# Performance work log

Measured on AMD Instinct MI355X. Metric: run time of the kernel, lower is better.

## Reference

```python
import jax, jax.numpy as jnp
import numpy as np

# ---- model hyperparameters (match init_kwargs) ----
D_MODEL = 1024
D_STATE = 128
EXPAND = 2
HEADDIM = 64
NGROUPS = 1
D_INNER = EXPAND * D_MODEL            # 2048
NHEADS = D_INNER // HEADDIM           # 32
ROPE_FRAC = 0.5
SPLIT = int(D_STATE * ROPE_FRAC)      # 64 rotary dims
NANG = SPLIT // 2                     # 32 rope angles
A_FLOOR = 1e-4
EPS = 1e-5
BATCH, SEQLEN = 1, 1024
SIZES = [D_INNER, D_INNER, D_STATE * NGROUPS, D_STATE * NGROUPS, NHEADS, NHEADS, NHEADS, NANG]
D_IN_PROJ = int(np.sum(SIZES))        # 4480


def setup_inputs() -> dict:
    key = jax.random.key(0)
    ks = jax.random.split(key, 6)
    u = jax.random.normal(ks[0], (BATCH, SEQLEN, D_MODEL), dtype=jnp.float32)
    W_in = jax.random.normal(ks[1], (D_MODEL, D_IN_PROJ), dtype=jnp.float32) * 0.02
    # dt_bias ~ log(dt) for dt in [1e-3, 0.1] -> around -4
    dt_bias = jax.random.normal(ks[2], (NHEADS,), dtype=jnp.float32) * 0.5 - 4.0
    B_bias = jnp.ones((NHEADS, D_STATE), jnp.float32) + 0.01 * jax.random.normal(ks[3], (NHEADS, D_STATE), dtype=jnp.float32)
    C_bias = jnp.ones((NHEADS, D_STATE), jnp.float32) + 0.01 * jax.random.normal(ks[4], (NHEADS, D_STATE), dtype=jnp.float32)
    Bn_w = jnp.ones((D_STATE,), jnp.float32)
    Cn_w = jnp.ones((D_STATE,), jnp.float32)
    D_param = jnp.ones((NHEADS,), jnp.float32)
    W_out = jax.random.normal(ks[5], (D_INNER, D_MODEL), dtype=jnp.float32) * 0.02
    return {"u": u, "W_in": W_in, "dt_bias": dt_bias, "B_bias": B_bias, "C_bias": C_bias,
            "Bn_w": Bn_w, "Cn_w": Cn_w, "D_param": D_param, "W_out": W_out}


def _rmsnorm(v, w):
    return v * jax.lax.rsqrt(jnp.mean(v * v, axis=-1, keepdims=True) + EPS) * w


def _forward(u, W_in, dt_bias, B_bias, C_bias, Bn_w, Cn_w, D_param, W_out):
    b, l, _ = u.shape
    proj = u @ W_in                                   # (b, l, d_in_proj)
    idx = np.cumsum(SIZES)[:-1]
    z, x, Bp, Cp, dd_dt, dd_A, trap_raw, ang = jnp.split(proj, idx, axis=-1)
    z = z.reshape(b, l, NHEADS, HEADDIM)
    x = x.reshape(b, l, NHEADS, HEADDIM)
    # A = clamp(-softplus(.), max=-A_floor);  dt = softplus(. + dt_bias)
    A = jnp.minimum(-jax.nn.softplus(dd_A), -A_FLOOR)          # (b,l,H)
    dt = jax.nn.softplus(dd_dt + dt_bias)                      # (b,l,H)
    a = jnp.exp(A * dt)                                        # decay per step
    lam = jax.nn.sigmoid(trap_raw)                             # trapezoid gate
    # RMSNorm on B/C (ngroups=1), then per-head additive bias
    Bn = _rmsnorm(Bp, Bn_w)                                    # (b,l,N)
    Cn = _rmsnorm(Cp, Cn_w)
    Bh = Bn[:, :, None, :] + B_bias                            # (b,l,H,N)
    Ch = Cn[:, :, None, :] + C_bias
    # data-dependent rotary: cumulative angle = cumsum(angles * dt)
    theta = jnp.cumsum(ang[:, :, None, :] * dt[..., None], axis=1)  # (b,l,H,NANG)
    cos, sin = jnp.cos(theta), jnp.sin(theta)

    def rope(v):
        d1, d2, rest = v[..., :NANG], v[..., NANG:SPLIT], v[..., SPLIT:]
        return jnp.concatenate([d1 * cos - d2 * sin, d1 * sin + d2 * cos, rest], axis=-1)

    Bh, Ch = rope(Bh), rope(Ch)

    tfirst = lambda v: jnp.moveaxis(v, 1, 0)
    inputs = (tfirst(Bh), tfirst(Ch), tfirst(x), tfirst(a), tfirst(dt), tfirst(lam))
    h0 = jnp.zeros((b, NHEADS, HEADDIM, D_STATE), jnp.float32)
    k0 = jnp.zeros((b, NHEADS, D_STATE), jnp.float32)
    v0 = jnp.zeros((b, NHEADS, HEADDIM), jnp.float32)

    def step(carry, inp):
        h, kp, vp = carry
        Bt, Ct, xt, at, dtt, lamt = inp
        # trapezoidal selective-scan update:
        # h_t = a_t h_{t-1} + dt_t (lam_t B_t x_t + (1-lam_t) a_t B_{t-1} x_{t-1})
        cur = jnp.einsum('bhp,bhn->bhpn', xt, Bt) * (dtt * lamt)[..., None, None]
        prv = jnp.einsum('bhp,bhn->bhpn', vp, kp) * (dtt * (1.0 - lamt) * at)[..., None, None]
        h = at[..., None, None] * h + cur + prv
        yt = jnp.einsum('bhn,bhpn->bhp', Ct, h)
        return (h, Bt, xt), yt

    _, y = jax.lax.scan(step, (h0, k0, v0), inputs)          # (l,b,H,P)
    y = jnp.moveaxis(y, 0, 1) + D_param[None, None, :, None] * x
    y = y * jax.nn.silu(z)                                    # gated output (no out-proj norm)
    return y.reshape(b, l, D_INNER) @ W_out


def reference(u, W_in, dt_bias, B_bias, C_bias, Bn_w, Cn_w, D_param, W_out):
    return _forward(u, W_in, dt_bias, B_bias, C_bias, Bn_w, Cn_w, D_param, W_out)
```

## Files before the change

kernel.cpp:

```cpp
#include <hip/hip_runtime.h>
#include <stdint.h>

#define SEQ     1024
#define DPROJ   4480

typedef __attribute__((ext_vector_type(8))) short short8;
typedef __attribute__((ext_vector_type(4))) float f4;

__device__ __forceinline__ short f2b(float f){
  union { float f; uint32_t u; } v; v.f = f;
  uint32_t r = (v.u + 0x7fffu + ((v.u >> 16) & 1u)) >> 16;
  return (short)(uint16_t)r;
}
__device__ __forceinline__ float b2f(uint16_t u){
  union { uint32_t u; float f; } v; v.u = ((uint32_t)u) << 16; return v.f;
}
__device__ __forceinline__ uint32_t pack2(float lo, float hi){
  return (uint32_t)(uint16_t)f2b(lo) | ((uint32_t)(uint16_t)f2b(hi) << 16);
}
__device__ __forceinline__ float softplus_f(float x){
  return x > 20.f ? x : log1pf(__expf(x));
}
__device__ __forceinline__ void gload_lds16(const short* g, short* l){
  __builtin_amdgcn_global_load_lds((const __attribute__((address_space(1))) void*)g,
                                   (__attribute__((address_space(3))) void*)l, 16, 0, 0);
}

__global__ __launch_bounds__(256) void cast_kernel(const float* __restrict__ in, short* __restrict__ out){
  int i = (blockIdx.x * 256 + threadIdx.x) * 4;
  f4 v = *(const f4*)(in + i);
  uint2 pk; pk.x = pack2(v.x, v.y); pk.y = pack2(v.z, v.w);
  *(uint2*)(out + i) = pk;
}

__global__ __launch_bounds__(256) void transpose_cast(const float* __restrict__ in, short* __restrict__ out,
                                                      int R, int C, int lda, int c0){
  __shared__ float tile[32][33];
  int bc = blockIdx.x * 32;
  int br = blockIdx.y * 32;
  int tx = threadIdx.x, ty = threadIdx.y;
  #pragma unroll
  for (int i = 0; i < 32; i += 8)
    tile[ty + i][tx] = in[(size_t)(br + ty + i) * lda + c0 + bc + tx];
  __syncthreads();
  #pragma unroll
  for (int i = 0; i < 32; i += 8)
    out[(size_t)(bc + ty + i) * R + br + tx] = f2b(tile[tx][ty + i]);
}

__global__ __launch_bounds__(256) void gemm_bt(const short* __restrict__ A, const short* __restrict__ Bt,
                                               float* __restrict__ C, int M, int N, int K, int klen){
  __shared__ __align__(16) short As[128 * 32];
  __shared__ __align__(16) short Bs[128 * 32];
  const int tid  = threadIdx.x;
  const int wave = tid >> 6;
  const int lane = tid & 63;
  const int m0 = blockIdx.y * 128;
  const int n0 = blockIdx.x * 128;
  const int k0 = blockIdx.z * klen;
  C += (size_t)blockIdx.z * M * N;
  const int wm = (wave >> 1) * 64;
  const int wn = (wave & 1) * 64;
  const int quad = lane >> 4;
  const int r16  = lane & 15;

  f4 acc[4][4];
  #pragma unroll
  for (int i = 0; i < 4; i++)
    #pragma unroll
    for (int j = 0; j < 4; j++) acc[i][j] = (f4){0.f, 0.f, 0.f, 0.f};

  const int row0 = tid >> 2;
  const int kq   = tid & 3;
  const short* gA0 = A  + (size_t)(m0 + row0) * K + k0 + kq * 8;
  const short* gA1 = A  + (size_t)(m0 + row0 + 64) * K + k0 + kq * 8;
  const short* gB0 = Bt + (size_t)(n0 + row0) * K + k0 + kq * 8;
  const short* gB1 = Bt + (size_t)(n0 + row0 + 64) * K + k0 + kq * 8;
  short* lA0 = &As[(size_t)tid * 8];
  short* lA1 = &As[(size_t)(tid + 256) * 8];
  short* lB0 = &Bs[(size_t)tid * 8];
  short* lB1 = &Bs[(size_t)(tid + 256) * 8];

  const int nk = klen >> 5;
  for (int kt = 0; kt < nk; ++kt){
    const int ko = kt * 32;
    __syncthreads();
    gload_lds16(gA0 + ko, lA0);
    gload_lds16(gA1 + ko, lA1);
    gload_lds16(gB0 + ko, lB0);
    gload_lds16(gB1 + ko, lB1);
    __syncthreads();
    short8 af[4], bf[4];
    #pragma unroll
    for (int i = 0; i < 4; i++){
      af[i] = *(const short8*)&As[(wm + i * 16 + r16) * 32 + quad * 8];
      bf[i] = *(const short8*)&Bs[(wn + i * 16 + r16) * 32 + quad * 8];
    }
    #pragma unroll
    for (int i = 0; i < 4; i++)
      #pragma unroll
      for (int j = 0; j < 4; j++)
        acc[i][j] = __builtin_amdgcn_mfma_f32_16x16x32_bf16(af[i], bf[j], acc[i][j], 0, 0, 0);
  }

  #pragma unroll
  for (int i = 0; i < 4; i++)
    #pragma unroll
    for (int j = 0; j < 4; j++)
      #pragma unroll
      for (int rr = 0; rr < 4; ++rr){
        int row = m0 + wm + i * 16 + quad * 4 + rr;
        int col = n0 + wn + j * 16 + r16;
        C[(size_t)row * N + col] = acc[i][j][rr];
      }
}

__global__ __launch_bounds__(256) void reduce4_kernel(const float* __restrict__ p, float* __restrict__ out){
  int i = (blockIdx.x * 256 + threadIdx.x) * 4;
  f4 a = *(const f4*)(p + i);
  f4 b = *(const f4*)(p + 1048576 + i);
  f4 c = *(const f4*)(p + 2097152 + i);
  f4 d = *(const f4*)(p + 3145728 + i);
  f4 s; s.x = (a.x + b.x) + (c.x + d.x); s.y = (a.y + b.y) + (c.y + d.y);
  s.z = (a.z + b.z) + (c.z + d.z); s.w = (a.w + b.w) + (c.w + d.w);
  *(f4*)(out + i) = s;
}

__global__ __launch_bounds__(256) void prep_kernel(const float* __restrict__ proj,
                                                   const float* __restrict__ dt_bias,
                                                   f4* __restrict__ coefA){
  int idx = blockIdx.x * 256 + threadIdx.x;
  int t = idx >> 5, h = idx & 31;
  const float* row = proj + (size_t)t * DPROJ;
  float dt  = softplus_f(row[4352 + h] + dt_bias[h]);
  float Ah  = -fmaxf(softplus_f(row[4384 + h]), 1e-4f);
  float lam = 1.f / (1.f + __expf(-row[4416 + h]));
  f4 c; c.x = Ah * dt; c.y = dt * lam; c.z = dt * (1.f - lam); c.w = dt;
  coefA[idx] = c;
}

__global__ __launch_bounds__(256) void scanL_kernel(const f4* __restrict__ coefA,
                                                    float* __restrict__ Lcum,
                                                    float* __restrict__ u2b,
                                                    float* __restrict__ c1b){
  int h = blockIdx.x;
  int tid = threadIdx.x;
  int t0 = tid * 4;
  float v[4], c1[4], c2n[4];
  #pragma unroll
  for (int i = 0; i < 4; i++){
    f4 cc = coefA[(t0 + i) * 32 + h];
    v[i] = cc.x; c1[i] = cc.y;
  }
  #pragma unroll
  for (int i = 0; i < 4; i++){
    int t = t0 + i;
    c2n[i] = (t < 1023) ? coefA[(t + 1) * 32 + h].z : 0.f;
  }
  v[1] += v[0]; v[2] += v[1]; v[3] += v[2];
  float tot = v[3], sc = tot;
  int lane = tid & 63, wave = tid >> 6;
  #pragma unroll
  for (int off = 1; off < 64; off <<= 1){
    float n = __shfl_up(sc, off, 64);
    if (lane >= off) sc += n;
  }
  __shared__ float wsum[4];
  if (lane == 63) wsum[wave] = sc;
  __syncthreads();
  float base = sc - tot;
  for (int w = 0; w < wave; ++w) base += wsum[w];
  #pragma unroll
  for (int i = 0; i < 4; i++){
    int t = t0 + i;
    Lcum[h * 1024 + t] = base + v[i];
    u2b[h * 1024 + t]  = c1[i] + c2n[i];
    c1b[h * 1024 + t]  = c1[i];
  }
}

__global__ __launch_bounds__(256) void theta2_kernel(const float* __restrict__ proj,
                                                     const f4* __restrict__ coefA,
                                                     float* __restrict__ cosb, float* __restrict__ sinb){
  int h = blockIdx.x >> 5, k = blockIdx.x & 31;
  int tid = threadIdx.x;
  int t0 = tid * 4;
  float v[4];
  #pragma unroll
  for (int i = 0; i < 4; i++){
    int t = t0 + i;
    v[i] = proj[(size_t)t * DPROJ + 4448 + k] * coefA[t * 32 + h].w;
  }
  v[1] += v[0]; v[2] += v[1]; v[3] += v[2];
  float tot = v[3], sc = tot;
  int lane = tid & 63, wave = tid >> 6;
  #pragma unroll
  for (int off = 1; off < 64; off <<= 1){
    float n = __shfl_up(sc, off, 64);
    if (lane >= off) sc += n;
  }
  __shared__ float wsum[4];
  if (lane == 63) wsum[wave] = sc;
  __syncthreads();
  float base = sc - tot;
  for (int w = 0; w < wave; ++w) base += wsum[w];
  #pragma unroll
  for (int i = 0; i < 4; i++){
    float th = base + v[i];
    float s, c;
    __sincosf(th, &s, &c);
    int t = t0 + i;
    cosb[(size_t)t * 1024 + h * 32 + k] = c;
    sinb[(size_t)t * 1024 + h * 32 + k] = s;
  }
}

__global__ __launch_bounds__(256) void bc_kernel(const float* __restrict__ proj,
                                                 const float* __restrict__ B_bias, const float* __restrict__ C_bias,
                                                 const float* __restrict__ Bn_w, const float* __restrict__ Cn_w,
                                                 const float* __restrict__ cosb, const float* __restrict__ sinb,
                                                 short* __restrict__ Bb, short* __restrict__ Cb){
  int t = blockIdx.x;
  int tid = threadIdx.x;
  __shared__ float vB[128], vC[128];
  __shared__ float red[4];
  int n = tid & 127;
  bool isC = tid >= 128;
  float val = proj[(size_t)t * DPROJ + 4096 + (isC ? 128 : 0) + n];
  float ss = val * val;
  #pragma unroll
  for (int off = 32; off >= 1; off >>= 1) ss += __shfl_down(ss, off);
  int wave = tid >> 6, lane = tid & 63;
  if (lane == 0) red[wave] = ss;
  __syncthreads();
  float rsv = isC ? rsqrtf((red[2] + red[3]) * (1.f / 128.f) + 1e-5f)
                  : rsqrtf((red[0] + red[1]) * (1.f / 128.f) + 1e-5f);
  float nv = val * rsv * (isC ? Cn_w[n] : Bn_w[n]);
  (isC ? vC : vB)[n] = nv;
  __syncthreads();
  const float* bias = isC ? C_bias : B_bias;
  const float* base = isC ? vC : vB;
  short* outp = isC ? Cb : Bb;
  const float* cb = cosb + (size_t)t * 1024;
  const float* sb = sinb + (size_t)t * 1024;
  for (int h = 0; h < 32; ++h){
    float v = base[n] + bias[h * 128 + n];
    float o;
    if (n < 32){
      float v2 = base[n + 32] + bias[h * 128 + n + 32];
      float c = cb[h * 32 + n], s = sb[h * 32 + n];
      o = v * c - v2 * s;
    } else if (n < 64){
      int k = n - 32;
      float v1 = base[k] + bias[h * 128 + k];
      float c = cb[h * 32 + k], s = sb[h * 32 + k];
      o = v1 * s + v * c;
    } else {
      o = v;
    }
    outp[(size_t)t * 4096 + h * 128 + n] = f2b(o);
  }
}

__global__ __launch_bounds__(256) void hpart_kernel(const short* __restrict__ xTb, const short* __restrict__ Bb,
                                                    const float* __restrict__ Lcum, const float* __restrict__ u2b,
                                                    short* __restrict__ Hpart){
  int h = blockIdx.x >> 3, c = blockIdx.x & 7;
  int t0 = c * 128;
  int tid = threadIdx.x;
  __shared__ float wS[128];
  if (tid < 128){
    float Lend = Lcum[h * 1024 + t0 + 127];
    wS[tid] = __expf(Lend - Lcum[h * 1024 + t0 + tid]) * u2b[h * 1024 + t0 + tid];
  }
  __syncthreads();
  int wave = tid >> 6, lane = tid & 63, quad = lane >> 4, r16 = lane & 15;
  int n0 = wave * 32;
  f4 acc[4][2];
  #pragma unroll
  for (int i = 0; i < 4; i++)
    #pragma unroll
    for (int j = 0; j < 2; j++) acc[i][j] = (f4){0.f, 0.f, 0.f, 0.f};

  const ushort* Bh = (const ushort*)Bb + (size_t)t0 * 4096 + h * 128;
  #pragma unroll
  for (int kk = 0; kk < 4; ++kk){
    int sb = kk * 32 + quad * 8;
    short8 af[4];
    #pragma unroll
    for (int i = 0; i < 4; i++){
      int p = i * 16 + r16;
      af[i] = *(const short8*)(xTb + (size_t)(h * 64 + p) * 1024 + t0 + sb);
    }
    float wv[8];
    #pragma unroll
    for (int jj = 0; jj < 8; jj++) wv[jj] = wS[sb + jj];
    short8 bfr[2];
    #pragma unroll
    for (int j = 0; j < 2; j++){
      int n = n0 + j * 16 + r16;
      float e[8];
      #pragma unroll
      for (int jj = 0; jj < 8; jj++)
        e[jj] = b2f(Bh[(size_t)(sb + jj) * 4096 + n]) * wv[jj];
      union { short8 s; uint32_t u[4]; } fr;
      #pragma unroll
      for (int q = 0; q < 4; q++) fr.u[q] = pack2(e[2 * q], e[2 * q + 1]);
      bfr[j] = fr.s;
    }
    #pragma unroll
    for (int i = 0; i < 4; i++)
      #pragma unroll
      for (int j = 0; j < 2; j++)
        acc[i][j] = __builtin_amdgcn_mfma_f32_16x16x32_bf16(af[i], bfr[j], acc[i][j], 0, 0, 0);
  }

  short* out = Hpart + ((size_t)(h * 8 + c)) * 8192;
  #pragma unroll
  for (int i = 0; i < 4; i++)
    #pragma unroll
    for (int rr = 0; rr < 4; ++rr){
      int p = i * 16 + quad * 4 + rr;
      #pragma unroll
      for (int j = 0; j < 2; j++){
        int n = n0 + j * 16 + r16;
        out[p * 128 + n] = f2b(acc[i][j][rr]);
      }
    }
}

__global__ __launch_bounds__(256) void hscan_kernel(const short* __restrict__ Hpart,
                                                    const float* __restrict__ Lcum,
                                                    short* __restrict__ Hused){
  int idx = blockIdx.x * 256 + threadIdx.x;
  int h = idx >> 13, rem = idx & 8191;
  float acc = 0.f;
  float Lprev = 0.f;
  #pragma unroll
  for (int c = 0; c < 8; c++){
    Hused[((size_t)(h * 8 + c)) * 8192 + rem] = f2b(acc);
    float Lend = Lcum[h * 1024 + c * 128 + 127];
    float dec = __expf(Lend - Lprev);
    acc = dec * acc + b2f((uint16_t)Hpart[((size_t)(h * 8 + c)) * 8192 + rem]);
    Lprev = Lend;
  }
}

#define GS 144
__global__ __launch_bounds__(256) void chunky_kernel(const short* __restrict__ Cb, const short* __restrict__ Bbg,
                                                     const short* __restrict__ xTb, const short* __restrict__ Hused,
                                                     const float* __restrict__ Lcum, const float* __restrict__ u2b,
                                                     const float* __restrict__ c1b,
                                                     float* __restrict__ ybuf){
  int h = blockIdx.x >> 3, c = blockIdx.x & 7;
  int t0 = c * 128;
  __shared__ __align__(16) short Gt[128 * GS];
  __shared__ float Lc[128], u2v[128], c1v[128];
  int tid = threadIdx.x;
  if (tid < 128){
    Lc[tid]  = Lcum[h * 1024 + t0 + tid];
    u2v[tid] = u2b[h * 1024 + t0 + tid];
    c1v[tid] = c1b[h * 1024 + t0 + tid];
  }
  float Lprev = (c > 0) ? Lcum[h * 1024 + t0 - 1] : 0.f;
  int wave = tid >> 6, lane = tid & 63, quad = lane >> 4, r16 = lane & 15;
  int wm = (wave >> 1) * 64, wn = (wave & 1) * 64;

  f4 acc[4][4];
  #pragma unroll
  for (int i = 0; i < 4; i++)
    #pragma unroll
    for (int j = 0; j < 4; j++) acc[i][j] = (f4){0.f, 0.f, 0.f, 0.f};
  #pragma unroll
  for (int kk = 0; kk < 4; ++kk){
    short8 af[4], bf[4];
    #pragma unroll
    for (int i = 0; i < 4; i++)
      af[i] = *(const short8*)(Cb + (size_t)(t0 + wm + i * 16 + r16) * 4096 + h * 128 + kk * 32 + quad * 8);
    #pragma unroll
    for (int j = 0; j < 4; j++)
      bf[j] = *(const short8*)(Bbg + (size_t)(t0 + wn + j * 16 + r16) * 4096 + h * 128 + kk * 32 + quad * 8);
    #pragma unroll
    for (int i = 0; i < 4; i++)
      #pragma unroll
      for (int j = 0; j < 4; j++)
        acc[i][j] = __builtin_amdgcn_mfma_f32_16x16x32_bf16(af[i], bf[j], acc[i][j], 0, 0, 0);
  }
  __syncthreads();

  #pragma unroll
  for (int i = 0; i < 4; i++){
    #pragma unroll
    for (int rr = 0; rr < 4; ++rr){
      int trow = wm + i * 16 + quad * 4 + rr;
      float Lt = Lc[trow];
      #pragma unroll
      for (int j = 0; j < 4; j++){
        int scol = wn + j * 16 + r16;
        float g = 0.f;
        if (scol <= trow){
          float wcoef = (scol == trow) ? c1v[scol] : u2v[scol];
          g = acc[i][j][rr] * wcoef * __expf(Lt - Lc[scol]);
        }
        Gt[trow * GS + scol] = f2b(g);
      }
    }
  }
  __syncthreads();

  f4 accY[2][4], accZ[2][4];
  #pragma unroll
  for (int i = 0; i < 2; i++)
    #pragma unroll
    for (int j = 0; j < 4; j++){ accY[i][j] = (f4){0.f,0.f,0.f,0.f}; accZ[i][j] = (f4){0.f,0.f,0.f,0.f}; }
  int m0 = wave * 32;
  #pragma unroll
  for (int kk = 0; kk < 4; ++kk){
    short8 ag[2], ac[2], bx[4], bh[4];
    #pragma unroll
    for (int i = 0; i < 2; i++){
      ag[i] = *(const short8*)&Gt[(m0 + i * 16 + r16) * GS + kk * 32 + quad * 8];
      ac[i] = *(const short8*)(Cb + (size_t)(t0 + m0 + i * 16 + r16) * 4096 + h * 128 + kk * 32 + quad * 8);
    }
    #pragma unroll
    for (int j = 0; j < 4; j++){
      bx[j] = *(const short8*)(xTb + (size_t)(h * 64 + j * 16 + r16) * 1024 + t0 + kk * 32 + quad * 8);
      bh[j] = *(const short8*)(Hused + ((size_t)(h * 8 + c) * 64 + j * 16 + r16) * 128 + kk * 32 + quad * 8);
    }
    #pragma unroll
    for (int i = 0; i < 2; i++)
      #pragma unroll
      for (int j = 0; j < 4; j++){
        accY[i][j] = __builtin_amdgcn_mfma_f32_16x16x32_bf16(ag[i], bx[j], accY[i][j], 0, 0, 0);
        accZ[i][j] = __builtin_amdgcn_mfma_f32_16x16x32_bf16(ac[i], bh[j], accZ[i][j], 0, 0, 0);
      }
  }
  #pragma unroll
  for (int i = 0; i < 2; i++)
    #pragma unroll
    for (int rr = 0; rr < 4; ++rr){
      int trow = m0 + i * 16 + quad * 4 + rr;
      float ei = __expf(Lc[trow] - Lprev);
      #pragma unroll
      for (int j = 0; j < 4; j++){
        int p = j * 16 + r16;
        ybuf[(size_t)(t0 + trow) * 2048 + h * 64 + p] = accY[i][j][rr] + ei * accZ[i][j][rr];
      }
    }
}

__global__ __launch_bounds__(256) void post_kernel(const float* __restrict__ y, const float* __restrict__ proj,
                                                   const float* __restrict__ D_par, short* __restrict__ yb){
  int i = (blockIdx.x * 256 + threadIdx.x) * 4;
  int t = i >> 11, d = i & 2047;
  int h = d >> 6;
  f4 yv = *(const f4*)(y + i);
  f4 xv = *(const f4*)(proj + (size_t)t * DPROJ + 2048 + d);
  f4 zv = *(const f4*)(proj + (size_t)t * DPROJ + d);
  float Dp = D_par[h];
  float o0 = (yv.x + Dp * xv.x) * (zv.x / (1.f + __expf(-zv.x)));
  float o1 = (yv.y + Dp * xv.y) * (zv.y / (1.f + __expf(-zv.y)));
  float o2 = (yv.z + Dp * xv.z) * (zv.z / (1.f + __expf(-zv.z)));
  float o3 = (yv.w + Dp * xv.w) * (zv.w / (1.f + __expf(-zv.w)));
  uint2 pk; pk.x = pack2(o0, o1); pk.y = pack2(o2, o3);
  *(uint2*)(yb + i) = pk;
}

extern "C" void kernel_launch(void* const* d_in, const int* in_sizes, int n_in,
                              void* d_out, int out_size, void* d_ws, size_t ws_size,
                              hipStream_t stream){
  const float* u       = (const float*)d_in[0];
  const float* W_in    = (const float*)d_in[1];
  const float* dt_bias = (const float*)d_in[2];
  const float* B_bias  = (const float*)d_in[3];
  const float* C_bias  = (const float*)d_in[4];
  const float* Bn_w    = (const float*)d_in[5];
  const float* Cn_w    = (const float*)d_in[6];
  const float* D_par   = (const float*)d_in[7];
  const float* W_out   = (const float*)d_in[8];
  float* out = (float*)d_out;

  char* ws = (char*)d_ws;
  short* u16   = (short*)(ws + 0);
  short* WtIn  = (short*)(ws + 2097152);
  short* WtOut = (short*)(ws + 11272192);
  float* proj  = (float*)(ws + 15466496);
  f4*    coefA = (f4*)   (ws + 33816576);
  float* cosb  = (float*)(ws + 34340864);
  float* sinb  = (float*)(ws + 38535168);
  short* Bb    = (short*)(ws + 42729472);
  short* Cb    = (short*)(ws + 51118080);
  short* xTb   = (short*)(ws + 59506688);
  float* Lcum  = (float*)(ws + 63700992);
  float* u2b   = (float*)(ws + 63832064);
  float* c1b   = (float*)(ws + 63963136);
  short* Hpart = (short*)(ws + 64094208);
  short* Hused = (short*)(ws + 68288512);
  float* ybuf  = (float*)(ws + 72482816);
  short* yb16  = (short*)(ws + 80871424);
  float* part  = proj;

  cast_kernel<<<1024, 256, 0, stream>>>(u, u16);
  transpose_cast<<<dim3(140, 32), dim3(32, 8), 0, stream>>>(W_in, WtIn, 1024, 4480, 4480, 0);
  transpose_cast<<<dim3(32, 64), dim3(32, 8), 0, stream>>>(W_out, WtOut, 2048, 1024, 1024, 0);
  gemm_bt<<<dim3(35, 8, 1), 256, 0, stream>>>(u16, WtIn, proj, 1024, 4480, 1024, 1024);
  prep_kernel<<<128, 256, 0, stream>>>(proj, dt_bias, coefA);
  scanL_kernel<<<32, 256, 0, stream>>>(coefA, Lcum, u2b, c1b);
  theta2_kernel<<<1024, 256, 0, stream>>>(proj, coefA, cosb, sinb);
  bc_kernel<<<1024, 256, 0, stream>>>(proj, B_bias, C_bias, Bn_w, Cn_w, cosb, sinb, Bb, Cb);
  transpose_cast<<<dim3(64, 32), dim3(32, 8), 0, stream>>>(proj, xTb, 1024, 2048, 4480, 2048);
  hpart_kernel<<<256, 256, 0, stream>>>(xTb, Bb, Lcum, u2b, Hpart);
  hscan_kernel<<<1024, 256, 0, stream>>>(Hpart, Lcum, Hused);
  chunky_kernel<<<256, 256, 0, stream>>>(Cb, Bb, xTb, Hused, Lcum, u2b, c1b, ybuf);
  post_kernel<<<2048, 256, 0, stream>>>(ybuf, proj, D_par, yb16);
  gemm_bt<<<dim3(8, 8, 4), 256, 0, stream>>>(yb16, WtOut, part, 1024, 1024, 2048, 512);
  reduce4_kernel<<<1024, 256, 0, stream>>>(part, out);
}
```

Measured before the change: 238.7 us.

## Fuse prep/post kernels, atomic split-K output, retile GEMM1 and transposes

Several changes land together. The prep kernel is folded into the scan, and the post (gating) step is fused into the chunk-output kernel. The final split-K GEMM accumulates with atomics into a zeroed output instead of using a separate reduce pass. GEMM1 uses 128x160 tiles so the grid covers the columns with 28 blocks. The transpose-cast kernels use larger tiles with vectorized bf16 stores, and bc_kernel is vectorized. The aim is to cut launches and intermediate memory traffic, at the cost of float atomics making the output order nondeterministic.

```diff
diff --git a/kernel.cpp b/kernel.cpp
--- a/kernel.cpp
+++ b/kernel.cpp
@@ -35,21 +35,100 @@
 
 __global__ __launch_bounds__(256) void transpose_cast(const float* __restrict__ in, short* __restrict__ out,
                                                       int R, int C, int lda, int c0){
-  __shared__ float tile[32][33];
+  __shared__ float tile[32][132];
   int bc = blockIdx.x * 32;
-  int br = blockIdx.y * 32;
-  int tx = threadIdx.x, ty = threadIdx.y;
-  #pragma unroll
-  for (int i = 0; i < 32; i += 8)
-    tile[ty + i][tx] = in[(size_t)(br + ty + i) * lda + c0 + bc + tx];
-  __syncthreads();
-  #pragma unroll
-  for (int i = 0; i < 32; i += 8)
-    out[(size_t)(bc + ty + i) * R + br + tx] = f2b(tile[tx][ty + i]);
-}
-
-__global__ __launch_bounds__(256) void gemm_bt(const short* __restrict__ A, const short* __restrict__ Bt,
-                                               float* __restrict__ C, int M, int N, int K, int klen){
+  int br = blockIdx.y * 128;
+  int tid = threadIdx.x;
+  int c = tid & 31, r0 = tid >> 5;
+  #pragma unroll
+  for (int i = 0; i < 16; i++){
+    int r = r0 + i * 8;
+    tile[c][r] = in[(size_t)(br + r) * lda + c0 + bc + c];
+  }
+  __syncthreads();
+  #pragma unroll
+  for (int i = 0; i < 4; i++){
+    int task = tid + 256 * i;
+    int cc = task >> 5;
+    int rg = (task & 31) * 4;
+    f4 v = *(const f4*)&tile[cc][rg];
+    uint2 pk; pk.x = pack2(v.x, v.y); pk.y = pack2(v.z, v.w);
+    *(uint2*)(out + (size_t)(bc + cc) * R + br + rg) = pk;
+  }
+}
+
+__global__ __launch_bounds__(256) void gemm1_kernel(const short* __restrict__ A, const short* __restrict__ Bt,
+                                                    float* __restrict__ C){
+  const int M = 1024, N = 4480, K = 1024;
+  __shared__ __align__(16) short As[128 * 32];
+  __shared__ __align__(16) short Bs[160 * 32];
+  const int tid  = threadIdx.x;
+  const int wave = tid >> 6;
+  const int lane = tid & 63;
+  const int m0 = blockIdx.y * 128;
+  const int n0 = blockIdx.x * 160;
+  const int wm = (wave >> 1) * 64;
+  const int wn = (wave & 1) * 80;
+  const int quad = lane >> 4;
+  const int r16  = lane & 15;
+
+  f4 acc[4][5];
+  #pragma unroll
+  for (int i = 0; i < 4; i++)
+    #pragma unroll
+    for (int j = 0; j < 5; j++) acc[i][j] = (f4){0.f, 0.f, 0.f, 0.f};
+
+  const int row0 = tid >> 2;
+  const int kq   = tid & 3;
+  const short* gA0 = A  + (size_t)(m0 + row0) * K + kq * 8;
+  const short* gA1 = A  + (size_t)(m0 + row0 + 64) * K + kq * 8;
+  const short* gB0 = Bt + (size_t)(n0 + row0) * K + kq * 8;
+  const short* gB1 = Bt + (size_t)(n0 + row0 + 64) * K + kq * 8;
+  const short* gB2 = Bt + (size_t)(n0 + row0 + 128) * K + kq * 8;
+  short* lA0 = &As[(size_t)tid * 8];
+  short* lA1 = &As[(size_t)(tid + 256) * 8];
+  short* lB0 = &Bs[(size_t)tid * 8];
+  short* lB1 = &Bs[(size_t)(tid + 256) * 8];
+  short* lB2 = &Bs[(size_t)(tid + 512) * 8];
+
+  for (int kt = 0; kt < 32; ++kt){
+    const int ko = kt * 32;
+    __syncthreads();
+    gload_lds16(gA0 + ko, lA0);
+    gload_lds16(gA1 + ko, lA1);
+    gload_lds16(gB0 + ko, lB0);
+    gload_lds16(gB1 + ko, lB1);
+    if (tid < 128) gload_lds16(gB2 + ko, lB2);
+    __syncthreads();
+    short8 af[4], bf[5];
+    #pragma unroll
+    for (int i = 0; i < 4; i++)
+      af[i] = *(const short8*)&As[(wm + i * 16 + r16) * 32 + quad * 8];
+    #pragma unroll
+    for (int j = 0; j < 5; j++)
+      bf[j] = *(const short8*)&Bs[(wn + j * 16 + r16) * 32 + quad * 8];
+    #pragma unroll
+    for (int i = 0; i < 4; i++)
+      #pragma unroll
+      for (int j = 0; j < 5; j++)
+        acc[i][j] = __builtin_amdgcn_mfma_f32_16x16x32_bf16(af[i], bf[j], acc[i][j], 0, 0, 0);
+  }
+
+  #pragma unroll
+  for (int i = 0; i < 4; i++)
+    #pragma unroll
+    for (int j = 0; j < 5; j++)
+      #pragma unroll
+      for (int rr = 0; rr < 4; ++rr){
+        int row = m0 + wm + i * 16 + quad * 4 + rr;
+        int col = n0 + wn + j * 16 + r16;
+        C[(size_t)row * N + col] = acc[i][j][rr];
+      }
+}
+
+__global__ __launch_bounds__(256) void gemm2_kernel(const short* __restrict__ A, const short* __restrict__ Bt,
+                                                    float* __restrict__ C){
+  const int N = 1024, K = 2048, klen = 512;
   __shared__ __align__(16) short As[128 * 32];
   __shared__ __align__(16) short Bs[128 * 32];
   const int tid  = threadIdx.x;
@@ -58,7 +137,6 @@
   const int m0 = blockIdx.y * 128;
   const int n0 = blockIdx.x * 128;
   const int k0 = blockIdx.z * klen;
-  C += (size_t)blockIdx.z * M * N;
   const int wm = (wave >> 1) * 64;
   const int wn = (wave & 1) * 64;
   const int quad = lane >> 4;
@@ -81,8 +159,7 @@
   short* lB0 = &Bs[(size_t)tid * 8];
   short* lB1 = &Bs[(size_t)(tid + 256) * 8];
 
-  const int nk = klen >> 5;
-  for (int kt = 0; kt < nk; ++kt){
+  for (int kt = 0; kt < klen / 32; ++kt){
     const int ko = kt * 32;
     __syncthreads();
     gload_lds16(gA0 + ko, lA0);
@@ -111,51 +188,37 @@
       for (int rr = 0; rr < 4; ++rr){
         int row = m0 + wm + i * 16 + quad * 4 + rr;
         int col = n0 + wn + j * 16 + r16;
-        C[(size_t)row * N + col] = acc[i][j][rr];
+        unsafeAtomicAdd(&C[(size_t)row * N + col], acc[i][j][rr]);
       }
 }
 
-__global__ __launch_bounds__(256) void reduce4_kernel(const float* __restrict__ p, float* __restrict__ out){
-  int i = (blockIdx.x * 256 + threadIdx.x) * 4;
-  f4 a = *(const f4*)(p + i);
-  f4 b = *(const f4*)(p + 1048576 + i);
-  f4 c = *(const f4*)(p + 2097152 + i);
-  f4 d = *(const f4*)(p + 3145728 + i);
-  f4 s; s.x = (a.x + b.x) + (c.x + d.x); s.y = (a.y + b.y) + (c.y + d.y);
-  s.z = (a.z + b.z) + (c.z + d.z); s.w = (a.w + b.w) + (c.w + d.w);
-  *(f4*)(out + i) = s;
-}
-
-__global__ __launch_bounds__(256) void prep_kernel(const float* __restrict__ proj,
-                                                   const float* __restrict__ dt_bias,
-                                                   f4* __restrict__ coefA){
-  int idx = blockIdx.x * 256 + threadIdx.x;
-  int t = idx >> 5, h = idx & 31;
-  const float* row = proj + (size_t)t * DPROJ;
-  float dt  = softplus_f(row[4352 + h] + dt_bias[h]);
-  float Ah  = -fmaxf(softplus_f(row[4384 + h]), 1e-4f);
-  float lam = 1.f / (1.f + __expf(-row[4416 + h]));
-  f4 c; c.x = Ah * dt; c.y = dt * lam; c.z = dt * (1.f - lam); c.w = dt;
-  coefA[idx] = c;
-}
-
-__global__ __launch_bounds__(256) void scanL_kernel(const f4* __restrict__ coefA,
-                                                    float* __restrict__ Lcum,
-                                                    float* __restrict__ u2b,
-                                                    float* __restrict__ c1b){
+__global__ __launch_bounds__(256) void scanL_kernel(const float* __restrict__ proj,
+                                                    const float* __restrict__ dt_bias,
+                                                    float* __restrict__ Lcum, float* __restrict__ u2b,
+                                                    float* __restrict__ c1b, float* __restrict__ dtb){
   int h = blockIdx.x;
   int tid = threadIdx.x;
   int t0 = tid * 4;
+  float dtbias = dt_bias[h];
+  float dt5[5], lam5[5];
+  #pragma unroll
+  for (int i = 0; i < 5; i++){
+    int t = t0 + i;
+    if (t < 1024){
+      const float* row = proj + (size_t)t * DPROJ;
+      dt5[i]  = softplus_f(row[4352 + h] + dtbias);
+      lam5[i] = 1.f / (1.f + __expf(-row[4416 + h]));
+    } else { dt5[i] = 0.f; lam5[i] = 0.f; }
+  }
   float v[4], c1[4], c2n[4];
-  #pragma unroll
-  for (int i = 0; i < 4; i++){
-    f4 cc = coefA[(t0 + i) * 32 + h];
-    v[i] = cc.x; c1[i] = cc.y;
-  }
   #pragma unroll
   for (int i = 0; i < 4; i++){
     int t = t0 + i;
-    c2n[i] = (t < 1023) ? coefA[(t + 1) * 32 + h].z : 0.f;
+    const float* row = proj + (size_t)t * DPROJ;
+    float Ah = -fmaxf(softplus_f(row[4384 + h]), 1e-4f);
+    v[i]   = Ah * dt5[i];
+    c1[i]  = dt5[i] * lam5[i];
+    c2n[i] = dt5[i + 1] * (1.f - lam5[i + 1]);
   }
   v[1] += v[0]; v[2] += v[1]; v[3] += v[2];
   float tot = v[3], sc = tot;
@@ -176,21 +239,21 @@
     Lcum[h * 1024 + t] = base + v[i];
     u2b[h * 1024 + t]  = c1[i] + c2n[i];
     c1b[h * 1024 + t]  = c1[i];
+    dtb[h * 1024 + t]  = dt5[i];
   }
 }
 
 __global__ __launch_bounds__(256) void theta2_kernel(const float* __restrict__ proj,
-                                                     const f4* __restrict__ coefA,
+                                                     const float* __restrict__ dtb,
                                                      float* __restrict__ cosb, float* __restrict__ sinb){
   int h = blockIdx.x >> 5, k = blockIdx.x & 31;
   int tid = threadIdx.x;
   int t0 = tid * 4;
+  f4 dtv = *(const f4*)&dtb[h * 1024 + t0];
   float v[4];
   #pragma unroll
-  for (int i = 0; i < 4; i++){
-    int t = t0 + i;
-    v[i] = proj[(size_t)t * DPROJ + 4448 + k] * coefA[t * 32 + h].w;
-  }
+  for (int i = 0; i < 4; i++)
+    v[i] = proj[(size_t)(t0 + i) * DPROJ + 4448 + k] * dtv[i];
   v[1] += v[0]; v[2] += v[1]; v[3] += v[2];
   float tot = v[3], sc = tot;
   int lane = tid & 63, wave = tid >> 6;
@@ -222,11 +285,11 @@
                                                  short* __restrict__ Bb, short* __restrict__ Cb){
   int t = blockIdx.x;
   int tid = threadIdx.x;
-  __shared__ float vB[128], vC[128];
+  __shared__ float vv[2][128];
   __shared__ float red[4];
   int n = tid & 127;
-  bool isC = tid >= 128;
-  float val = proj[(size_t)t * DPROJ + 4096 + (isC ? 128 : 0) + n];
+  int isC = tid >> 7;
+  float val = proj[(size_t)t * DPROJ + 4096 + isC * 128 + n];
   float ss = val * val;
   #pragma unroll
   for (int off = 32; off >= 1; off >>= 1) ss += __shfl_down(ss, off);
@@ -235,30 +298,44 @@
   __syncthreads();
   float rsv = isC ? rsqrtf((red[2] + red[3]) * (1.f / 128.f) + 1e-5f)
                   : rsqrtf((red[0] + red[1]) * (1.f / 128.f) + 1e-5f);
-  float nv = val * rsv * (isC ? Cn_w[n] : Bn_w[n]);
-  (isC ? vC : vB)[n] = nv;
-  __syncthreads();
-  const float* bias = isC ? C_bias : B_bias;
-  const float* base = isC ? vC : vB;
-  short* outp = isC ? Cb : Bb;
+  vv[isC][n] = val * rsv * (isC ? Cn_w[n] : Bn_w[n]);
+  __syncthreads();
   const float* cb = cosb + (size_t)t * 1024;
   const float* sb = sinb + (size_t)t * 1024;
-  for (int h = 0; h < 32; ++h){
-    float v = base[n] + bias[h * 128 + n];
-    float o;
-    if (n < 32){
-      float v2 = base[n + 32] + bias[h * 128 + n + 32];
-      float c = cb[h * 32 + n], s = sb[h * 32 + n];
-      o = v * c - v2 * s;
-    } else if (n < 64){
-      int k = n - 32;
-      float v1 = base[k] + bias[h * 128 + k];
-      float c = cb[h * 32 + k], s = sb[h * 32 + k];
-      o = v1 * s + v * c;
+  #pragma unroll
+  for (int it = 0; it < 8; it++){
+    int task = tid + 256 * it;
+    int arr  = task >> 10;
+    int rem  = task & 1023;
+    int h    = rem >> 5;
+    int n0   = (rem & 31) * 4;
+    const float* bias = arr ? C_bias : B_bias;
+    const float* base = vv[arr];
+    f4 bv = *(const f4*)&base[n0];
+    f4 bi = *(const f4*)&bias[h * 128 + n0];
+    f4 o;
+    if (n0 < 32){
+      f4 bv2 = *(const f4*)&base[n0 + 32];
+      f4 bi2 = *(const f4*)&bias[h * 128 + n0 + 32];
+      f4 cv = *(const f4*)&cb[h * 32 + n0];
+      f4 sv = *(const f4*)&sb[h * 32 + n0];
+      #pragma unroll
+      for (int q = 0; q < 4; q++) o[q] = (bv[q] + bi[q]) * cv[q] - (bv2[q] + bi2[q]) * sv[q];
+    } else if (n0 < 64){
+      int k0 = n0 - 32;
+      f4 bv1 = *(const f4*)&base[k0];
+      f4 bi1 = *(const f4*)&bias[h * 128 + k0];
+      f4 cv = *(const f4*)&cb[h * 32 + k0];
+      f4 sv = *(const f4*)&sb[h * 32 + k0];
+      #pragma unroll
+      for (int q = 0; q < 4; q++) o[q] = (bv1[q] + bi1[q]) * sv[q] + (bv[q] + bi[q]) * cv[q];
     } else {
-      o = v;
-    }
-    outp[(size_t)t * 4096 + h * 128 + n] = f2b(o);
+      #pragma unroll
+      for (int q = 0; q < 4; q++) o[q] = bv[q] + bi[q];
+    }
+    uint2 pk; pk.x = pack2(o.x, o.y); pk.y = pack2(o.z, o.w);
+    short* outp = arr ? Cb : Bb;
+    *(uint2*)(outp + (size_t)t * 4096 + h * 128 + n0) = pk;
   }
 }
 
@@ -298,11 +375,11 @@
     short8 bfr[2];
     #pragma unroll
     for (int j = 0; j < 2; j++){
-      int n = n0 + j * 16 + r16;
+      int nn = n0 + j * 16 + r16;
       float e[8];
       #pragma unroll
       for (int jj = 0; jj < 8; jj++)
-        e[jj] = b2f(Bh[(size_t)(sb + jj) * 4096 + n]) * wv[jj];
+        e[jj] = b2f(Bh[(size_t)(sb + jj) * 4096 + nn]) * wv[jj];
       union { short8 s; uint32_t u[4]; } fr;
       #pragma unroll
       for (int q = 0; q < 4; q++) fr.u[q] = pack2(e[2 * q], e[2 * q + 1]);
@@ -323,8 +400,8 @@
       int p = i * 16 + quad * 4 + rr;
       #pragma unroll
       for (int j = 0; j < 2; j++){
-        int n = n0 + j * 16 + r16;
-        out[p * 128 + n] = f2b(acc[i][j][rr]);
+        int nn = n0 + j * 16 + r16;
+        out[p * 128 + nn] = f2b(acc[i][j][rr]);
       }
     }
 }
@@ -351,7 +428,8 @@
                                                      const short* __restrict__ xTb, const short* __restrict__ Hused,
                                                      const float* __restrict__ Lcum, const float* __restrict__ u2b,
                                                      const float* __restrict__ c1b,
-                                                     float* __restrict__ ybuf){
+                                                     const float* __restrict__ proj, const float* __restrict__ D_par,
+                                                     short* __restrict__ yb16){
   int h = blockIdx.x >> 3, c = blockIdx.x & 7;
   int t0 = c * 128;
   __shared__ __align__(16) short Gt[128 * GS];
@@ -363,6 +441,7 @@
     c1v[tid] = c1b[h * 1024 + t0 + tid];
   }
   float Lprev = (c > 0) ? Lcum[h * 1024 + t0 - 1] : 0.f;
+  float Dp = D_par[h];
   int wave = tid >> 6, lane = tid & 63, quad = lane >> 4, r16 = lane & 15;
   int wm = (wave >> 1) * 64, wn = (wave & 1) * 64;
 
@@ -441,29 +520,17 @@
     for (int rr = 0; rr < 4; ++rr){
       int trow = m0 + i * 16 + quad * 4 + rr;
       float ei = __expf(Lc[trow] - Lprev);
+      const float* prow = proj + (size_t)(t0 + trow) * DPROJ;
       #pragma unroll
       for (int j = 0; j < 4; j++){
-        int p = j * 16 + r16;
-        ybuf[(size_t)(t0 + trow) * 2048 + h * 64 + p] = accY[i][j][rr] + ei * accZ[i][j][rr];
+        int col = h * 64 + j * 16 + r16;
+        float zv = prow[col];
+        float xv = prow[2048 + col];
+        float yv = accY[i][j][rr] + ei * accZ[i][j][rr] + Dp * xv;
+        float o = yv * (zv / (1.f + __expf(-zv)));
+        yb16[(size_t)(t0 + trow) * 2048 + col] = f2b(o);
       }
     }
-}
-
-__global__ __launch_bounds__(256) void post_kernel(const float* __restrict__ y, const float* __restrict__ proj,
-                                                   const float* __restrict__ D_par, short* __restrict__ yb){
-  int i = (blockIdx.x * 256 + threadIdx.x) * 4;
-  int t = i >> 11, d = i & 2047;
-  int h = d >> 6;
-  f4 yv = *(const f4*)(y + i);
-  f4 xv = *(const f4*)(proj + (size_t)t * DPROJ + 2048 + d);
-  f4 zv = *(const f4*)(proj + (size_t)t * DPROJ + d);
-  float Dp = D_par[h];
-  float o0 = (yv.x + Dp * xv.x) * (zv.x / (1.f + __expf(-zv.x)));
-  float o1 = (yv.y + Dp * xv.y) * (zv.y / (1.f + __expf(-zv.y)));
-  float o2 = (yv.z + Dp * xv.z) * (zv.z / (1.f + __expf(-zv.z)));
-  float o3 = (yv.w + Dp * xv.w) * (zv.w / (1.f + __expf(-zv.w)));
-  uint2 pk; pk.x = pack2(o0, o1); pk.y = pack2(o2, o3);
-  *(uint2*)(yb + i) = pk;
 }
 
 extern "C" void kernel_launch(void* const* d_in, const int* in_sizes, int n_in,
@@ -485,34 +552,30 @@
   short* WtIn  = (short*)(ws + 2097152);
   short* WtOut = (short*)(ws + 11272192);
   float* proj  = (float*)(ws + 15466496);
-  f4*    coefA = (f4*)   (ws + 33816576);
-  float* cosb  = (float*)(ws + 34340864);
-  float* sinb  = (float*)(ws + 38535168);
-  short* Bb    = (short*)(ws + 42729472);
-  short* Cb    = (short*)(ws + 51118080);
-  short* xTb   = (short*)(ws + 59506688);
-  float* Lcum  = (float*)(ws + 63700992);
-  float* u2b   = (float*)(ws + 63832064);
-  float* c1b   = (float*)(ws + 63963136);
-  short* Hpart = (short*)(ws + 64094208);
-  short* Hused = (short*)(ws + 68288512);
-  float* ybuf  = (float*)(ws + 72482816);
-  short* yb16  = (short*)(ws + 80871424);
-  float* part  = proj;
-
+  float* cosb  = (float*)(ws + 33816576);
+  float* sinb  = (float*)(ws + 38010880);
+  short* Bb    = (short*)(ws + 42205184);
+  short* Cb    = (short*)(ws + 50593792);
+  short* xTb   = (short*)(ws + 58982400);
+  float* Lcum  = (float*)(ws + 63176704);
+  float* u2b   = (float*)(ws + 63307776);
+  float* c1b   = (float*)(ws + 63438848);
+  float* dtb   = (float*)(ws + 63569920);
+  short* Hpart = (short*)(ws + 63700992);
+  short* Hused = (short*)(ws + 67895296);
+  short* yb16  = (short*)(ws + 72089600);
+
+  hipMemsetAsync(out, 0, (size_t)out_size * sizeof(float), stream);
   cast_kernel<<<1024, 256, 0, stream>>>(u, u16);
-  transpose_cast<<<dim3(140, 32), dim3(32, 8), 0, stream>>>(W_in, WtIn, 1024, 4480, 4480, 0);
-  transpose_cast<<<dim3(32, 64), dim3(32, 8), 0, stream>>>(W_out, WtOut, 2048, 1024, 1024, 0);
-  gemm_bt<<<dim3(35, 8, 1), 256, 0, stream>>>(u16, WtIn, proj, 1024, 4480, 1024, 1024);
-  prep_kernel<<<128, 256, 0, stream>>>(proj, dt_bias, coefA);
-  scanL_kernel<<<32, 256, 0, stream>>>(coefA, Lcum, u2b, c1b);
-  theta2_kernel<<<1024, 256, 0, stream>>>(proj, coefA, cosb, sinb);
+  transpose_cast<<<dim3(140, 8), 256, 0, stream>>>(W_in, WtIn, 1024, 4480, 4480, 0);
+  transpose_cast<<<dim3(32, 16), 256, 0, stream>>>(W_out, WtOut, 2048, 1024, 1024, 0);
+  gemm1_kernel<<<dim3(28, 8), 256, 0, stream>>>(u16, WtIn, proj);
+  scanL_kernel<<<32, 256, 0, stream>>>(proj, dt_bias, Lcum, u2b, c1b, dtb);
+  theta2_kernel<<<1024, 256, 0, stream>>>(proj, dtb, cosb, sinb);
   bc_kernel<<<1024, 256, 0, stream>>>(proj, B_bias, C_bias, Bn_w, Cn_w, cosb, sinb, Bb, Cb);
-  transpose_cast<<<dim3(64, 32), dim3(32, 8), 0, stream>>>(proj, xTb, 1024, 2048, 4480, 2048);
+  transpose_cast<<<dim3(64, 8), 256, 0, stream>>>(proj, xTb, 1024, 2048, 4480, 2048);
   hpart_kernel<<<256, 256, 0, stream>>>(xTb, Bb, Lcum, u2b, Hpart);
   hscan_kernel<<<1024, 256, 0, stream>>>(Hpart, Lcum, Hused);
-  chunky_kernel<<<256, 256, 0, stream>>>(Cb, Bb, xTb, Hused, Lcum, u2b, c1b, ybuf);
-  post_kernel<<<2048, 256, 0, stream>>>(ybuf, proj, D_par, yb16);
-  gemm_bt<<<dim3(8, 8, 4), 256, 0, stream>>>(yb16, WtOut, part, 1024, 1024, 2048, 512);
-  reduce4_kernel<<<1024, 256, 0, stream>>>(part, out);
-}
+  chunky_kernel<<<256, 256, 0, stream>>>(Cb, Bb, xTb, Hused, Lcum, u2b, c1b, proj, D_par, yb16);
+  gemm2_kernel<<<dim3(8, 8, 4), 256, 0, stream>>>(yb16, WtOut, out);
+}
```

After: 218.9 us. 8.3% less time.
